# Kernel optimization log

Measured on AMD Instinct MI355X. Metric: run time of the kernel, lower is better.

## Reference

```python
import jax, jax.numpy as jnp
import numpy as np


def _lstm_cell(x, h, c, W_ih, W_hh, b_ih, b_hh):
    # torch.nn.LSTMCell: gates ordered (i, f, g, o)
    gates = x @ W_ih.T + h @ W_hh.T + b_ih + b_hh
    i, f, g, o = jnp.split(gates, 4, axis=-1)
    c_next = jax.nn.sigmoid(f) * c + jax.nn.sigmoid(i) * jnp.tanh(g)
    h_next = jax.nn.sigmoid(o) * jnp.tanh(c_next)
    return h_next, c_next


def setup_inputs() -> dict:
    key = jax.random.key(0)
    ks = jax.random.split(key, 6)
    B, T, N, K_SUP, E = 64, 128, 128, 8, 512
    scale = 1.0 / np.sqrt(E)
    return {
        "targets": jax.random.normal(ks[0], (B, T, E), jnp.float32),
        "support_embeddings": jax.random.normal(ks[1], (B, N, K_SUP, E), jnp.float32),
        "W_ih": jax.random.normal(ks[2], (4 * E, E), jnp.float32) * scale,
        "W_hh": jax.random.normal(ks[3], (4 * E, E), jnp.float32) * scale,
        "b_ih": jnp.zeros((4 * E,), jnp.float32),
        "b_hh": jnp.zeros((4 * E,), jnp.float32),
        "processing_steps": 10,
    }


def reference(targets, support_embeddings, W_ih, W_hh, b_ih, b_hh, processing_steps):
    B, T, E = targets.shape
    _, N, K_SUP, _ = support_embeddings.shape
    x = targets.reshape(B * T, E)  # flattened targets fed every step

    def step(carry, _):
        h_prev, c_prev = carry
        h_next, c_next = _lstm_cell(x, h_prev, c_prev, W_ih, W_hh, b_ih, b_hh)
        h_next = h_next + x  # residual add of the input encoding
        # attention scores between previous hidden state and support set
        hq = h_prev.reshape(B, T, E)
        scores = jnp.einsum('bte,bnke->btnk', hq, support_embeddings)
        attn = jax.nn.softmax(scores.reshape(B, T, N * K_SUP), axis=-1)
        attn = attn.reshape(B, T, N, K_SUP)
        # attention read over the support embeddings
        r = jnp.einsum('btnk,bnke->bte', attn, support_embeddings)
        h_next = h_next + r.reshape(B * T, E)
        return (h_next, c_next), None

    h0 = jnp.zeros_like(x)
    c0 = jnp.zeros_like(x)
    (h_fin, _), _ = jax.lax.scan(step, (h0, c0), None, length=processing_steps)
    return h_fin.reshape(B, T, E)
```

## Files before the change

### kernel.cpp

```cpp
#include <hip/hip_runtime.h>

#define DI __device__ __forceinline__
typedef unsigned short u16;
typedef __bf16 v8bf  __attribute__((ext_vector_type(8)));
typedef float  f32x4 __attribute__((ext_vector_type(4)));

DI u16 f2bf(float f){ unsigned u=__float_as_uint(f); return (u16)((u + 0x7fffu + ((u>>16)&1u))>>16); }
DI float bf2f(u16 u){ return __uint_as_float(((unsigned)u)<<16); }
DI float sigf(float x){ return 1.f/(1.f+__expf(-x)); }

DI void gload16(const void* g, void* l){
  __builtin_amdgcn_global_load_lds((const __attribute__((address_space(1))) unsigned int*)g,
                                   (__attribute__((address_space(3))) unsigned int*)l, 16, 0, 0);
}

DI void xswz(int& bx, int& by){
  int gx=gridDim.x, nwg=gx*gridDim.y;
  int bid=blockIdx.y*gx+blockIdx.x;
  int cpx=nwg>>3;
  int sw=(bid&7)*cpx+(bid>>3);
  bx=sw%gx; by=sw/gx;
}

DI void stage128(const u16* __restrict__ G, int ld, u16* Ls, int tid){
  #pragma unroll
  for(int j=0;j<4;++j){
    int ci=j*256+tid; int r=ci>>3, ch=ci&7;
    gload16(G + (size_t)r*ld + ((ch^(r&7))<<3), Ls + ci*8);
  }
}
DI void stage_gate(const u16* __restrict__ W, int e0, int k0, u16* Ls, int tid){
  #pragma unroll
  for(int j=0;j<4;++j){
    int ci=j*256+tid; int r=ci>>3, ch=ci&7;
    int row=((r>>4)&3)*512 + e0 + (r>>6)*16 + (r&15);
    gload16(W + (size_t)row*512 + k0 + ((ch^(r&7))<<3), Ls + ci*8);
  }
}

DI void kcompute(const u16* AhS,const u16* AlS,const u16* BhS,const u16* BlS,
                 f32x4 (&acc)[4][4], int wr,int wc,int l15,int kh){
  int r7=l15&7;
  int co0=((kh^r7)<<3), co1=(((4+kh)^r7)<<3);
  v8bf ah[4][2], al[4][2];
  #pragma unroll
  for(int mi=0;mi<4;++mi){
    int ro=(wr*64+mi*16+l15)*64;
    ah[mi][0]=*(const v8bf*)(AhS+ro+co0); ah[mi][1]=*(const v8bf*)(AhS+ro+co1);
    al[mi][0]=*(const v8bf*)(AlS+ro+co0); al[mi][1]=*(const v8bf*)(AlS+ro+co1);
  }
  #pragma unroll
  for(int n=0;n<4;++n){
    int ro=(wc*64+n*16+l15)*64;
    v8bf bh0=*(const v8bf*)(BhS+ro+co0), bh1=*(const v8bf*)(BhS+ro+co1);
    v8bf bl0=*(const v8bf*)(BlS+ro+co0), bl1=*(const v8bf*)(BlS+ro+co1);
    __builtin_amdgcn_s_setprio(1);
    #pragma unroll
    for(int mi=0;mi<4;++mi) acc[mi][n]=__builtin_amdgcn_mfma_f32_16x16x32_bf16(ah[mi][0],bh0,acc[mi][n],0,0,0);
    #pragma unroll
    for(int mi=0;mi<4;++mi) acc[mi][n]=__builtin_amdgcn_mfma_f32_16x16x32_bf16(ah[mi][1],bh1,acc[mi][n],0,0,0);
    #pragma unroll
    for(int mi=0;mi<4;++mi) acc[mi][n]=__builtin_amdgcn_mfma_f32_16x16x32_bf16(al[mi][0],bh0,acc[mi][n],0,0,0);
    #pragma unroll
    for(int mi=0;mi<4;++mi) acc[mi][n]=__builtin_amdgcn_mfma_f32_16x16x32_bf16(al[mi][1],bh1,acc[mi][n],0,0,0);
    #pragma unroll
    for(int mi=0;mi<4;++mi) acc[mi][n]=__builtin_amdgcn_mfma_f32_16x16x32_bf16(ah[mi][0],bl0,acc[mi][n],0,0,0);
    #pragma unroll
    for(int mi=0;mi<4;++mi) acc[mi][n]=__builtin_amdgcn_mfma_f32_16x16x32_bf16(ah[mi][1],bl1,acc[mi][n],0,0,0);
    __builtin_amdgcn_s_setprio(0);
  }
}

#define LDS_DECL \
  __shared__ __attribute__((aligned(16))) u16 AhS[128*64]; \
  __shared__ __attribute__((aligned(16))) u16 AlS[128*64]; \
  __shared__ __attribute__((aligned(16))) u16 BhS[128*64]; \
  __shared__ __attribute__((aligned(16))) u16 BlS[128*64];

#define ACC_INIT f32x4 acc[4][4]; \
  _Pragma("unroll") for(int i_=0;i_<4;i_++){ _Pragma("unroll") for(int n_=0;n_<4;n_++) acc[i_][n_]=(f32x4){0.f,0.f,0.f,0.f}; }

#define WAVE_IDS int tid=threadIdx.x, w=tid>>6, wr=w>>1, wc=w&1, lane=tid&63, l15=lane&15, kh=lane>>4; (void)lane;

#define KLOOP(NT, STG) \
  _Pragma("clang loop unroll(disable)") \
  for(int t=0;t<NT;++t){ \
    STG(t); \
    __syncthreads(); \
    kcompute(AhS,AlS,BhS,BlS,acc,wr,wc,l15,kh); \
    __syncthreads(); \
  }

__global__ void k_split(const float* __restrict__ in, u16* __restrict__ hi, u16* __restrict__ lo, int n4){
  int i=blockIdx.x*256+threadIdx.x;
  if(i<n4){
    float4 v=((const float4*)in)[i];
    ushort4 h,l;
    h.x=f2bf(v.x); l.x=f2bf(v.x-bf2f(h.x));
    h.y=f2bf(v.y); l.y=f2bf(v.y-bf2f(h.y));
    h.z=f2bf(v.z); l.z=f2bf(v.z-bf2f(h.z));
    h.w=f2bf(v.w); l.w=f2bf(v.w-bf2f(h.w));
    ((ushort4*)hi)[i]=h; ((ushort4*)lo)[i]=l;
  }
}

__global__ __launch_bounds__(256) void k_transpose(const float* __restrict__ U,
    u16* __restrict__ uth, u16* __restrict__ utl){
  __shared__ float T[64][65];
  int b=blockIdx.z, j0=blockIdx.y*64, e0=blockIdx.x*64;
  int tid=threadIdx.x;
  const float* Ub = U + ((size_t)b*1024 + j0)*512 + e0;
  #pragma unroll
  for(int it=0;it<16;++it){
    int idx=it*256+tid; int j=idx>>6, e=idx&63;
    T[j][e]=Ub[(size_t)j*512+e];
  }
  __syncthreads();
  size_t ob=((size_t)b*512 + e0)*1024 + j0;
  #pragma unroll
  for(int it=0;it<16;++it){
    int idx=it*256+tid; int e=idx>>6, j=idx&63;
    float v=T[j][e];
    u16 hb=f2bf(v);
    uth[ob+(size_t)e*1024+j]=hb;
    utl[ob+(size_t)e*1024+j]=f2bf(v-bf2f(hb));
  }
}

__global__ __launch_bounds__(256,2) void k_gx(const u16* __restrict__ xh, const u16* __restrict__ xl,
    const u16* __restrict__ wh, const u16* __restrict__ wl,
    const float* __restrict__ bih, const float* __restrict__ bhh,
    u16* __restrict__ gxh, u16* __restrict__ gxl)
{
  LDS_DECL
  int bx,by; xswz(bx,by);
  int n0=bx*128, m0=by*128;
  WAVE_IDS
  ACC_INIT
  const u16* Ah=xh+(size_t)m0*512; const u16* Al=xl+(size_t)m0*512;
  const u16* Bh=wh+(size_t)n0*512; const u16* Bl=wl+(size_t)n0*512;
  #define STG_GX(t) { int k0=(t)<<6; \
    stage128(Ah+k0,512,AhS,tid); stage128(Al+k0,512,AlS,tid); \
    stage128(Bh+k0,512,BhS,tid); stage128(Bl+k0,512,BlS,tid); }
  KLOOP(8, STG_GX)
  #pragma unroll
  for(int mi=0;mi<4;++mi){
    #pragma unroll
    for(int i=0;i<4;++i){
      int row=m0+wr*64+mi*16+kh*4+i;
      #pragma unroll
      for(int n=0;n<4;++n){
        int col=n0+wc*64+n*16+l15;
        float v=acc[mi][n][i]+bih[col]+bhh[col];
        u16 hb=f2bf(v);
        gxh[(size_t)row*2048+col]=hb;
        gxl[(size_t)row*2048+col]=f2bf(v-bf2f(hb));
      }
    }
  }
}

__global__ __launch_bounds__(256,2) void k_gates(const u16* __restrict__ hh, const u16* __restrict__ hl,
    const u16* __restrict__ whh_h, const u16* __restrict__ whh_l,
    const u16* __restrict__ gxh, const u16* __restrict__ gxl,
    const float* __restrict__ x, float* __restrict__ c, float* __restrict__ htmp)
{
  LDS_DECL
  int bx,by; xswz(bx,by);
  int e0=bx*32, m0=by*128;
  WAVE_IDS
  ACC_INIT
  const u16* Ah=hh+(size_t)m0*512; const u16* Al=hl+(size_t)m0*512;
  #define STG_GATES(t) { int k0=(t)<<6; \
    stage128(Ah+k0,512,AhS,tid); stage128(Al+k0,512,AlS,tid); \
    stage_gate(whh_h,e0,k0,BhS,tid); stage_gate(whh_l,e0,k0,BlS,tid); }
  KLOOP(8, STG_GATES)
  #pragma unroll
  for(int mi=0;mi<4;++mi){
    #pragma unroll
    for(int i=0;i<4;++i){
      int row=m0+wr*64+mi*16+kh*4+i;
      size_t gb=(size_t)row*2048;
      int e=e0+wc*16+l15;
      float gi=acc[mi][0][i]+bf2f(gxh[gb+e])     +bf2f(gxl[gb+e]);
      float gf=acc[mi][1][i]+bf2f(gxh[gb+512+e]) +bf2f(gxl[gb+512+e]);
      float gg=acc[mi][2][i]+bf2f(gxh[gb+1024+e])+bf2f(gxl[gb+1024+e]);
      float go=acc[mi][3][i]+bf2f(gxh[gb+1536+e])+bf2f(gxl[gb+1536+e]);
      size_t off=(size_t)row*512+e;
      float cn=sigf(gf)*c[off]+sigf(gi)*tanhf(gg);
      c[off]=cn;
      htmp[off]=sigf(go)*tanhf(cn)+x[off];
    }
  }
}

__global__ __launch_bounds__(256,2) void k_scores(const u16* __restrict__ hh, const u16* __restrict__ hl,
    const u16* __restrict__ uh, const u16* __restrict__ ul, float* __restrict__ S)
{
  LDS_DECL
  int bx,by; xswz(bx,by);
  int b=by, n0=bx*128, m0=b*128;
  WAVE_IDS
  ACC_INIT
  size_t ub=(size_t)b*1024*512+(size_t)n0*512;
  const u16* Ah=hh+(size_t)m0*512; const u16* Al=hl+(size_t)m0*512;
  const u16* Bh=uh+ub; const u16* Bl=ul+ub;
  #define STG_SC(t) { int k0=(t)<<6; \
    stage128(Ah+k0,512,AhS,tid); stage128(Al+k0,512,AlS,tid); \
    stage128(Bh+k0,512,BhS,tid); stage128(Bl+k0,512,BlS,tid); }
  KLOOP(8, STG_SC)
  #pragma unroll
  for(int mi=0;mi<4;++mi){
    #pragma unroll
    for(int i=0;i<4;++i){
      int row=m0+wr*64+mi*16+kh*4+i;
      #pragma unroll
      for(int n=0;n<4;++n)
        S[(size_t)row*1024 + n0+wc*64+n*16+l15]=acc[mi][n][i];
    }
  }
}

__global__ __launch_bounds__(256) void k_softmax(float* S){
  int row=blockIdx.x*4+(threadIdx.x>>6);
  int lane=threadIdx.x&63;
  float* sr=S+(size_t)row*1024;
  float4 v[4]; float m=-3.0e38f;
  #pragma unroll
  for(int i=0;i<4;++i){
    v[i]=((const float4*)sr)[i*64+lane];
    m=fmaxf(m,fmaxf(fmaxf(v[i].x,v[i].y),fmaxf(v[i].z,v[i].w)));
  }
  #pragma unroll
  for(int s=32;s;s>>=1) m=fmaxf(m,__shfl_xor(m,s));
  float sum=0.f; float pv[16];
  #pragma unroll
  for(int i=0;i<4;++i){
    pv[i*4+0]=__expf(v[i].x-m); pv[i*4+1]=__expf(v[i].y-m);
    pv[i*4+2]=__expf(v[i].z-m); pv[i*4+3]=__expf(v[i].w-m);
    sum+=pv[i*4+0]+pv[i*4+1]+pv[i*4+2]+pv[i*4+3];
  }
  #pragma unroll
  for(int s=32;s;s>>=1) sum+=__shfl_xor(sum,s);
  float inv=1.f/sum;
  u16* ar=(u16*)S + (size_t)row*2048;
  #pragma unroll
  for(int i=0;i<4;++i){
    ushort4 h,l;
    float p;
    p=pv[i*4+0]*inv; h.x=f2bf(p); l.x=f2bf(p-bf2f(h.x));
    p=pv[i*4+1]*inv; h.y=f2bf(p); l.y=f2bf(p-bf2f(h.y));
    p=pv[i*4+2]*inv; h.z=f2bf(p); l.z=f2bf(p-bf2f(h.z));
    p=pv[i*4+3]*inv; h.w=f2bf(p); l.w=f2bf(p-bf2f(h.w));
    *(ushort4*)(ar + i*256+lane*4)        = h;
    *(ushort4*)(ar + 1024 + i*256+lane*4) = l;
  }
}

__global__ __launch_bounds__(256,2) void k_rcomb(const u16* __restrict__ attn, const u16* __restrict__ uth,
    const u16* __restrict__ utl, const float* __restrict__ htmp, float* hout,
    u16* __restrict__ hh, u16* __restrict__ hl)
{
  LDS_DECL
  int bx,by; xswz(bx,by);
  int b=by, n0=bx*128, m0=b*128;
  WAVE_IDS
  ACC_INIT
  size_t ub=(size_t)b*512*1024+(size_t)n0*1024;
  const u16* Ah=attn+(size_t)m0*2048;
  const u16* Al=Ah+1024;
  const u16* Bh=uth+ub; const u16* Bl=utl+ub;
  #define STG_RC(t) { int k0=(t)<<6; \
    stage128(Ah+k0,2048,AhS,tid); stage128(Al+k0,2048,AlS,tid); \
    stage128(Bh+k0,1024,BhS,tid); stage128(Bl+k0,1024,BlS,tid); }
  KLOOP(16, STG_RC)
  #pragma unroll
  for(int mi=0;mi<4;++mi){
    #pragma unroll
    for(int i=0;i<4;++i){
      int row=m0+wr*64+mi*16+kh*4+i;
      #pragma unroll
      for(int n=0;n<4;++n){
        int e=n0+wc*64+n*16+l15;
        size_t off=(size_t)row*512+e;
        float v=htmp[off]+acc[mi][n][i];
        if(hout) hout[off]=v;
        u16 hb=f2bf(v);
        hh[off]=hb; hl[off]=f2bf(v-bf2f(hb));
      }
    }
  }
}

extern "C" void kernel_launch(void* const* d_in, const int* in_sizes, int n_in,
                              void* d_out, int out_size, void* d_ws, size_t ws_size,
                              hipStream_t stream)
{
  const float* x   = (const float*)d_in[0];
  const float* U   = (const float*)d_in[1];
  const float* wihf= (const float*)d_in[2];
  const float* whhf= (const float*)d_in[3];
  const float* bih = (const float*)d_in[4];
  const float* bhh = (const float*)d_in[5];

  const size_t MB=1048576;
  char* p=(char*)d_ws;
  u16*   u_hi =(u16*)(p+  0*MB);
  u16*   u_lo =(u16*)(p+ 64*MB);
  u16*   ut_hi=(u16*)(p+128*MB);
  u16*   ut_lo=(u16*)(p+192*MB);
  u16*   gx_hi=(u16*)(p+256*MB);
  u16*   gx_lo=(u16*)(p+288*MB);
  float* S    =(float*)(p+320*MB);
  u16*   xhi  =(u16*)(p+320*MB);
  u16*   xlo  =(u16*)(p+336*MB);
  float* c    =(float*)(p+352*MB);
  float* htmp =(float*)(p+368*MB);
  u16*   wihh =(u16*)(p+368*MB);
  u16*   wihl =(u16*)(p+370*MB);
  u16*   h_hi =(u16*)(p+384*MB);
  u16*   h_lo =(u16*)(p+392*MB);
  u16*   whhh =(u16*)(p+400*MB);
  u16*   whhl =(u16*)(p+402*MB);
  if (ws_size < 404*MB){
    hipMemsetAsync(d_out, 0x3F, (size_t)out_size*4, stream);
    return;
  }

  k_split<<<4096 ,256,0,stream>>>(x,    xhi,  xlo,  1048576);
  k_split<<<1024 ,256,0,stream>>>(wihf, wihh, wihl, 262144);
  k_split<<<1024 ,256,0,stream>>>(whhf, whhh, whhl, 262144);
  k_split<<<32768,256,0,stream>>>(U,    u_hi, u_lo, 8388608);
  k_transpose<<<dim3(8,16,64),256,0,stream>>>(U, ut_hi, ut_lo);
  k_gx<<<dim3(16,64),256,0,stream>>>(xhi, xlo, wihh, wihl, bih, bhh, gx_hi, gx_lo);
  hipMemsetAsync(c,    0, 16*MB, stream);
  hipMemsetAsync(h_hi, 0,  8*MB, stream);
  hipMemsetAsync(h_lo, 0,  8*MB, stream);

  for (int s=0;s<10;++s){
    k_gates  <<<dim3(16,64),256,0,stream>>>(h_hi,h_lo, whhh,whhl, gx_hi,gx_lo, x, c, htmp);
    k_scores <<<dim3(8,64) ,256,0,stream>>>(h_hi,h_lo, u_hi,u_lo, S);
    k_softmax<<<2048       ,256,0,stream>>>(S);
    k_rcomb  <<<dim3(4,64) ,256,0,stream>>>((const u16*)S, ut_hi,ut_lo, htmp,
                                            (s==9)?(float*)d_out:nullptr, h_hi,h_lo);
  }
}
```

Before: 2.238 ms.

## Double-buffer LDS staging with half-depth K tiles in all GEMM kernels

Switches the shared GEMM main loop from a single 64-deep K tile with load-sync-compute-sync to two 32-deep LDS buffers. The next tile's global-to-LDS loads are issued before computing the current tile, so memory latency can overlap MFMA work. The LDS swizzle is adapted to 4 chunks per row. This doubles the number of loop iterations and barriers, and each iteration has less compute to hide latency behind. LDS usage per block stays the same.

```diff
diff --git a/kernel.cpp b/kernel.cpp
--- a/kernel.cpp
+++ b/kernel.cpp
@@ -22,72 +22,66 @@
   bx=sw%gx; by=sw/gx;
 }
 
-DI void stage128(const u16* __restrict__ G, int ld, u16* Ls, int tid){
-  #pragma unroll
-  for(int j=0;j<4;++j){
-    int ci=j*256+tid; int r=ci>>3, ch=ci&7;
-    gload16(G + (size_t)r*ld + ((ch^(r&7))<<3), Ls + ci*8);
-  }
-}
-DI void stage_gate(const u16* __restrict__ W, int e0, int k0, u16* Ls, int tid){
-  #pragma unroll
-  for(int j=0;j<4;++j){
-    int ci=j*256+tid; int r=ci>>3, ch=ci&7;
+DI void stage32(const u16* __restrict__ G, int ld, u16* Ls, int tid){
+  #pragma unroll
+  for(int j=0;j<2;++j){
+    int ci=j*256+tid; int r=ci>>2, ch=ci&3;
+    gload16(G + (size_t)r*ld + ((ch^((r>>1)&3))<<3), Ls + ci*8);
+  }
+}
+DI void stage_gate32(const u16* __restrict__ W, int e0, int k0, u16* Ls, int tid){
+  #pragma unroll
+  for(int j=0;j<2;++j){
+    int ci=j*256+tid; int r=ci>>2, ch=ci&3;
     int row=((r>>4)&3)*512 + e0 + (r>>6)*16 + (r&15);
-    gload16(W + (size_t)row*512 + k0 + ((ch^(r&7))<<3), Ls + ci*8);
-  }
-}
-
-DI void kcompute(const u16* AhS,const u16* AlS,const u16* BhS,const u16* BlS,
-                 f32x4 (&acc)[4][4], int wr,int wc,int l15,int kh){
-  int r7=l15&7;
-  int co0=((kh^r7)<<3), co1=(((4+kh)^r7)<<3);
-  v8bf ah[4][2], al[4][2];
-  #pragma unroll
-  for(int mi=0;mi<4;++mi){
-    int ro=(wr*64+mi*16+l15)*64;
-    ah[mi][0]=*(const v8bf*)(AhS+ro+co0); ah[mi][1]=*(const v8bf*)(AhS+ro+co1);
-    al[mi][0]=*(const v8bf*)(AlS+ro+co0); al[mi][1]=*(const v8bf*)(AlS+ro+co1);
+    gload16(W + (size_t)row*512 + k0 + ((ch^((r>>1)&3))<<3), Ls + ci*8);
+  }
+}
+
+DI void kcompute32(const u16* AhS,const u16* AlS,const u16* BhS,const u16* BlS,
+                   f32x4 (&acc)[4][4], int wr,int wc,int l15,int kh){
+  int co=((kh ^ ((l15>>1)&3))<<3);
+  v8bf ah[4], al[4];
+  #pragma unroll
+  for(int mi=0;mi<4;++mi){
+    int ro=(wr*64+mi*16+l15)*32;
+    ah[mi]=*(const v8bf*)(AhS+ro+co);
+    al[mi]=*(const v8bf*)(AlS+ro+co);
   }
   #pragma unroll
   for(int n=0;n<4;++n){
-    int ro=(wc*64+n*16+l15)*64;
-    v8bf bh0=*(const v8bf*)(BhS+ro+co0), bh1=*(const v8bf*)(BhS+ro+co1);
-    v8bf bl0=*(const v8bf*)(BlS+ro+co0), bl1=*(const v8bf*)(BlS+ro+co1);
+    int ro=(wc*64+n*16+l15)*32;
+    v8bf bh=*(const v8bf*)(BhS+ro+co);
+    v8bf bl=*(const v8bf*)(BlS+ro+co);
     __builtin_amdgcn_s_setprio(1);
     #pragma unroll
-    for(int mi=0;mi<4;++mi) acc[mi][n]=__builtin_amdgcn_mfma_f32_16x16x32_bf16(ah[mi][0],bh0,acc[mi][n],0,0,0);
-    #pragma unroll
-    for(int mi=0;mi<4;++mi) acc[mi][n]=__builtin_amdgcn_mfma_f32_16x16x32_bf16(ah[mi][1],bh1,acc[mi][n],0,0,0);
-    #pragma unroll
-    for(int mi=0;mi<4;++mi) acc[mi][n]=__builtin_amdgcn_mfma_f32_16x16x32_bf16(al[mi][0],bh0,acc[mi][n],0,0,0);
-    #pragma unroll
-    for(int mi=0;mi<4;++mi) acc[mi][n]=__builtin_amdgcn_mfma_f32_16x16x32_bf16(al[mi][1],bh1,acc[mi][n],0,0,0);
-    #pragma unroll
-    for(int mi=0;mi<4;++mi) acc[mi][n]=__builtin_amdgcn_mfma_f32_16x16x32_bf16(ah[mi][0],bl0,acc[mi][n],0,0,0);
-    #pragma unroll
-    for(int mi=0;mi<4;++mi) acc[mi][n]=__builtin_amdgcn_mfma_f32_16x16x32_bf16(ah[mi][1],bl1,acc[mi][n],0,0,0);
+    for(int mi=0;mi<4;++mi) acc[mi][n]=__builtin_amdgcn_mfma_f32_16x16x32_bf16(ah[mi],bh,acc[mi][n],0,0,0);
+    #pragma unroll
+    for(int mi=0;mi<4;++mi) acc[mi][n]=__builtin_amdgcn_mfma_f32_16x16x32_bf16(al[mi],bh,acc[mi][n],0,0,0);
+    #pragma unroll
+    for(int mi=0;mi<4;++mi) acc[mi][n]=__builtin_amdgcn_mfma_f32_16x16x32_bf16(ah[mi],bl,acc[mi][n],0,0,0);
     __builtin_amdgcn_s_setprio(0);
   }
 }
 
 #define LDS_DECL \
-  __shared__ __attribute__((aligned(16))) u16 AhS[128*64]; \
-  __shared__ __attribute__((aligned(16))) u16 AlS[128*64]; \
-  __shared__ __attribute__((aligned(16))) u16 BhS[128*64]; \
-  __shared__ __attribute__((aligned(16))) u16 BlS[128*64];
+  __shared__ __attribute__((aligned(16))) u16 AhS[2][128*32]; \
+  __shared__ __attribute__((aligned(16))) u16 AlS[2][128*32]; \
+  __shared__ __attribute__((aligned(16))) u16 BhS[2][128*32]; \
+  __shared__ __attribute__((aligned(16))) u16 BlS[2][128*32];
 
 #define ACC_INIT f32x4 acc[4][4]; \
   _Pragma("unroll") for(int i_=0;i_<4;i_++){ _Pragma("unroll") for(int n_=0;n_<4;n_++) acc[i_][n_]=(f32x4){0.f,0.f,0.f,0.f}; }
 
 #define WAVE_IDS int tid=threadIdx.x, w=tid>>6, wr=w>>1, wc=w&1, lane=tid&63, l15=lane&15, kh=lane>>4; (void)lane;
 
-#define KLOOP(NT, STG) \
+#define KLOOP2(NT, STG) \
+  STG(0,0); \
+  __syncthreads(); \
   _Pragma("clang loop unroll(disable)") \
   for(int t=0;t<NT;++t){ \
-    STG(t); \
-    __syncthreads(); \
-    kcompute(AhS,AlS,BhS,BlS,acc,wr,wc,l15,kh); \
+    if(t+1<NT) STG(t+1,(t+1)&1); \
+    kcompute32(AhS[t&1],AlS[t&1],BhS[t&1],BlS[t&1],acc,wr,wc,l15,kh); \
     __syncthreads(); \
   }
 
@@ -139,10 +133,10 @@
   ACC_INIT
   const u16* Ah=xh+(size_t)m0*512; const u16* Al=xl+(size_t)m0*512;
   const u16* Bh=wh+(size_t)n0*512; const u16* Bl=wl+(size_t)n0*512;
-  #define STG_GX(t) { int k0=(t)<<6; \
-    stage128(Ah+k0,512,AhS,tid); stage128(Al+k0,512,AlS,tid); \
-    stage128(Bh+k0,512,BhS,tid); stage128(Bl+k0,512,BlS,tid); }
-  KLOOP(8, STG_GX)
+  #define STG_GX(t,bb) { int k0=(t)<<5; \
+    stage32(Ah+k0,512,AhS[bb],tid); stage32(Al+k0,512,AlS[bb],tid); \
+    stage32(Bh+k0,512,BhS[bb],tid); stage32(Bl+k0,512,BlS[bb],tid); }
+  KLOOP2(16, STG_GX)
   #pragma unroll
   for(int mi=0;mi<4;++mi){
     #pragma unroll
@@ -171,10 +165,10 @@
   WAVE_IDS
   ACC_INIT
   const u16* Ah=hh+(size_t)m0*512; const u16* Al=hl+(size_t)m0*512;
-  #define STG_GATES(t) { int k0=(t)<<6; \
-    stage128(Ah+k0,512,AhS,tid); stage128(Al+k0,512,AlS,tid); \
-    stage_gate(whh_h,e0,k0,BhS,tid); stage_gate(whh_l,e0,k0,BlS,tid); }
-  KLOOP(8, STG_GATES)
+  #define STG_GATES(t,bb) { int k0=(t)<<5; \
+    stage32(Ah+k0,512,AhS[bb],tid); stage32(Al+k0,512,AlS[bb],tid); \
+    stage_gate32(whh_h,e0,k0,BhS[bb],tid); stage_gate32(whh_l,e0,k0,BlS[bb],tid); }
+  KLOOP2(16, STG_GATES)
   #pragma unroll
   for(int mi=0;mi<4;++mi){
     #pragma unroll
@@ -205,10 +199,10 @@
   size_t ub=(size_t)b*1024*512+(size_t)n0*512;
   const u16* Ah=hh+(size_t)m0*512; const u16* Al=hl+(size_t)m0*512;
   const u16* Bh=uh+ub; const u16* Bl=ul+ub;
-  #define STG_SC(t) { int k0=(t)<<6; \
-    stage128(Ah+k0,512,AhS,tid); stage128(Al+k0,512,AlS,tid); \
-    stage128(Bh+k0,512,BhS,tid); stage128(Bl+k0,512,BlS,tid); }
-  KLOOP(8, STG_SC)
+  #define STG_SC(t,bb) { int k0=(t)<<5; \
+    stage32(Ah+k0,512,AhS[bb],tid); stage32(Al+k0,512,AlS[bb],tid); \
+    stage32(Bh+k0,512,BhS[bb],tid); stage32(Bl+k0,512,BlS[bb],tid); }
+  KLOOP2(16, STG_SC)
   #pragma unroll
   for(int mi=0;mi<4;++mi){
     #pragma unroll
@@ -270,10 +264,10 @@
   const u16* Ah=attn+(size_t)m0*2048;
   const u16* Al=Ah+1024;
   const u16* Bh=uth+ub; const u16* Bl=utl+ub;
-  #define STG_RC(t) { int k0=(t)<<6; \
-    stage128(Ah+k0,2048,AhS,tid); stage128(Al+k0,2048,AlS,tid); \
-    stage128(Bh+k0,1024,BhS,tid); stage128(Bl+k0,1024,BlS,tid); }
-  KLOOP(16, STG_RC)
+  #define STG_RC(t,bb) { int k0=(t)<<5; \
+    stage32(Ah+k0,2048,AhS[bb],tid); stage32(Al+k0,2048,AlS[bb],tid); \
+    stage32(Bh+k0,1024,BhS[bb],tid); stage32(Bl+k0,1024,BlS[bb],tid); }
+  KLOOP2(32, STG_RC)
   #pragma unroll
   for(int mi=0;mi<4;++mi){
     #pragma unroll
```

Result: slower. 2.405 ms (+7.5%).
